# Performance work log

Hardware: AMD Instinct MI355X
Metric: run time of the kernel (lower is better)

The kernel has to match this reference:

```python
import jax, jax.numpy as jnp
import numpy as np

N = 100000
E = 1600000
IN_DIM = 128
OUT_DIM = 128


def setup_inputs() -> dict:
    key = jax.random.key(0)
    k1, k2, k3, k4, k5 = jax.random.split(key, 5)
    x = jax.random.normal(k1, (N, IN_DIM), dtype=jnp.float32)
    edge_index = jax.random.randint(k2, (2, E), 0, N, dtype=jnp.int64)
    # LayerNorm affine params
    ln_w = jnp.ones((IN_DIM,), dtype=jnp.float32)
    ln_b = jnp.zeros((IN_DIM,), dtype=jnp.float32)
    # SAGEConv params: lin_l (neighbor agg, with bias), lin_r (root, no bias)
    s = 1.0 / np.sqrt(IN_DIM)
    W_l = jax.random.uniform(k3, (OUT_DIM, IN_DIM), dtype=jnp.float32, minval=-s, maxval=s)
    b_l = jax.random.uniform(k4, (OUT_DIM,), dtype=jnp.float32, minval=-s, maxval=s)
    W_r = jax.random.uniform(k5, (OUT_DIM, IN_DIM), dtype=jnp.float32, minval=-s, maxval=s)
    return {"x": x, "edge_index": edge_index, "ln_w": ln_w, "ln_b": ln_b,
            "W_l": W_l, "b_l": b_l, "W_r": W_r}


def _layer_norm(x, w, b, eps=1e-5):
    mu = jnp.mean(x, axis=-1, keepdims=True)
    var = jnp.mean(jnp.square(x - mu), axis=-1, keepdims=True)
    return (x - mu) * jax.lax.rsqrt(var + eps) * w + b


def reference(x, edge_index, ln_w, ln_b, W_l, b_l, W_r):
    # norm -> activation -> dropout(p=0, identity)
    h = jax.nn.relu(_layer_norm(x, ln_w, ln_b))  # [N, in_dim]
    src = edge_index[0]  # message sources (x_j)
    dst = edge_index[1]  # aggregation targets
    # mean aggregation of neighbor features onto target nodes
    agg = jax.ops.segment_sum(h[src], dst, num_segments=N)  # [N, in_dim]
    cnt = jax.ops.segment_sum(jnp.ones((E,), dtype=h.dtype), dst, num_segments=N)
    agg = agg / jnp.maximum(cnt, 1.0)[:, None]
    # SAGEConv: lin_l(agg) + lin_r(h)
    out = agg @ W_l.T + b_l + h @ W_r.T  # [N, out_dim]
    return out
```

## Files before the change

### kernel.cpp

```cpp
#include <hip/hip_runtime.h>

#define N_NODES 100000
#define E_EDGES 1600000
#define DIM     128

#define NB1     196
#define CHUNK   8192
#define NBINS   512
#define NBUCKET 391
#define NBH     (NBINS * NB1)
#define HS_BLOCKS 98

#define HB_OFF    0
#define WTB_OFF   25600000
#define OFFS_OFF  25665536
#define BH_OFF    26065600
#define BSUM_OFF  26467008
#define BIN_OFF   26468032
#define SRC_OFF   32868032

typedef __attribute__((ext_vector_type(8))) short short8;
typedef __attribute__((ext_vector_type(4))) float floatx4;

__device__ __forceinline__ unsigned bf16pack(float a, float b) {
  unsigned ua = __float_as_uint(a); ua += 0x7fffu + ((ua >> 16) & 1u);
  unsigned ub = __float_as_uint(b); ub += 0x7fffu + ((ub >> 16) & 1u);
  return (ua >> 16) | (ub & 0xffff0000u);
}
__device__ __forceinline__ float2 bf16unpack(unsigned p) {
  return make_float2(__uint_as_float(p << 16), __uint_as_float(p & 0xffff0000u));
}

__global__ __launch_bounds__(256) void k_prep(const float* __restrict__ x,
                                              const float* __restrict__ lw,
                                              const float* __restrict__ lb,
                                              const float* __restrict__ Wl,
                                              const float* __restrict__ Wr,
                                              const int* __restrict__ ei,
                                              unsigned* __restrict__ hb,
                                              unsigned* __restrict__ wtb,
                                              int* __restrict__ bh) {
  int gid = blockIdx.x * 256 + threadIdx.x;
  int t = threadIdx.x;

  {
    int row  = blockIdx.x * 4 + (t >> 6);
    int lane = t & 63;
    float2 v = ((const float2*)(x + (size_t)row * DIM))[lane];
    float s  = v.x + v.y;
    float sq = v.x * v.x + v.y * v.y;
    #pragma unroll
    for (int off = 32; off > 0; off >>= 1) {
      s  += __shfl_xor(s, off);
      sq += __shfl_xor(sq, off);
    }
    float mu  = s * (1.0f / 128.0f);
    float var = sq * (1.0f / 128.0f) - mu * mu;
    float rs  = rsqrtf(var + 1e-5f);
    float2 w = ((const float2*)lw)[lane];
    float2 b = ((const float2*)lb)[lane];
    float ox = fmaxf((v.x - mu) * rs * w.x + b.x, 0.0f);
    float oy = fmaxf((v.y - mu) * rs * w.y + b.y, 0.0f);
    hb[(size_t)row * 64 + lane] = bf16pack(ox, oy);
  }

  if (gid < 16384) {
    int j2 = gid & 3;
    int q  = (gid >> 2) & 3;
    int c  = (gid >> 4) & 127;
    int kb = gid >> 11;
    int k0 = kb * 32 + q * 8 + j2 * 2;
    int k1 = k0 + 1;
    float v0 = (k0 < 128) ? Wl[c * 128 + k0] : Wr[c * 128 + (k0 - 128)];
    float v1 = (k1 < 128) ? Wl[c * 128 + k1] : Wr[c * 128 + (k1 - 128)];
    wtb[gid] = bf16pack(v0, v1);
  }

  if (blockIdx.x < NB1) {
    __shared__ int h[NBINS];
    h[t] = 0; h[t + 256] = 0;
    __syncthreads();
    const int4* d4p = (const int4*)(ei + E_EDGES);
    #pragma unroll
    for (int u = 0; u < 8; ++u) {
      int i4 = blockIdx.x * (CHUNK / 4) + u * 256 + t;
      if (i4 < E_EDGES / 4) {
        int4 d = d4p[i4];
        atomicAdd(&h[d.x >> 8], 1);
        atomicAdd(&h[d.y >> 8], 1);
        atomicAdd(&h[d.z >> 8], 1);
        atomicAdd(&h[d.w >> 8], 1);
      }
    }
    __syncthreads();
    bh[t * NB1 + blockIdx.x] = h[t];
    bh[(t + 256) * NB1 + blockIdx.x] = h[t + 256];
  }
}

__global__ __launch_bounds__(256) void k_hscan1(int* __restrict__ bh,
                                                int* __restrict__ bsum) {
  __shared__ int s[256];
  int t = threadIdx.x;
  int base = blockIdx.x * 1024 + t * 4;
  int a0 = (base + 0 < NBH) ? bh[base + 0] : 0;
  int a1 = (base + 1 < NBH) ? bh[base + 1] : 0;
  int a2 = (base + 2 < NBH) ? bh[base + 2] : 0;
  int a3 = (base + 3 < NBH) ? bh[base + 3] : 0;
  s[t] = a0 + a1 + a2 + a3;
  __syncthreads();
  #pragma unroll
  for (int off = 1; off < 256; off <<= 1) {
    int x = (t >= off) ? s[t - off] : 0;
    __syncthreads();
    s[t] += x;
    __syncthreads();
  }
  int excl = (t > 0) ? s[t - 1] : 0;
  if (t == 255) bsum[blockIdx.x] = s[255];
  if (base + 0 < NBH) bh[base + 0] = excl;
  if (base + 1 < NBH) bh[base + 1] = excl + a0;
  if (base + 2 < NBH) bh[base + 2] = excl + a0 + a1;
  if (base + 3 < NBH) bh[base + 3] = excl + a0 + a1 + a2;
}

__global__ __launch_bounds__(256) void k_hscan2(int* __restrict__ bh,
                                                const int* __restrict__ bsum) {
  __shared__ int s[256];
  int t = threadIdx.x;
  s[t] = (t < HS_BLOCKS) ? bsum[t] : 0;
  __syncthreads();
  #pragma unroll
  for (int off = 1; off < 256; off <<= 1) {
    int x = (t >= off) ? s[t - off] : 0;
    __syncthreads();
    s[t] += x;
    __syncthreads();
  }
  int blk = blockIdx.x;
  int add = (blk > 0) ? s[blk - 1] : 0;
  #pragma unroll
  for (int u = 0; u < 4; ++u) {
    int i = blk * 1024 + t * 4 + u;
    if (i < NBH) bh[i] += add;
  }
}

__global__ __launch_bounds__(256) void k_binsort(const int* __restrict__ ei,
                                                 const int* __restrict__ bh,
                                                 int* __restrict__ binned) {
  __shared__ int stage[CHUNK];
  __shared__ int addr[CHUNK];
  __shared__ int hist[NBINS];
  __shared__ int ebase[NBINS];
  __shared__ int cur[NBINS];
  __shared__ int gbase[NBINS];
  __shared__ int s[256];
  int t  = threadIdx.x;
  int ch = blockIdx.x;

  hist[t] = 0; hist[t + 256] = 0;
  gbase[t] = bh[t * NB1 + ch];
  gbase[t + 256] = bh[(t + 256) * NB1 + ch];
  __syncthreads();

  const int4* s4p = (const int4*)ei;
  const int4* d4p = (const int4*)(ei + E_EDGES);

  #pragma unroll
  for (int u = 0; u < 8; ++u) {
    int i4 = ch * (CHUNK / 4) + u * 256 + t;
    if (i4 < E_EDGES / 4) {
      int4 d = d4p[i4];
      atomicAdd(&hist[d.x >> 8], 1);
      atomicAdd(&hist[d.y >> 8], 1);
      atomicAdd(&hist[d.z >> 8], 1);
      atomicAdd(&hist[d.w >> 8], 1);
    }
  }
  __syncthreads();

  int h0 = hist[2 * t], h1 = hist[2 * t + 1];
  s[t] = h0 + h1;
  __syncthreads();
  #pragma unroll
  for (int off = 1; off < 256; off <<= 1) {
    int xv = (t >= off) ? s[t - off] : 0;
    __syncthreads();
    s[t] += xv;
    __syncthreads();
  }
  int ex = (t > 0) ? s[t - 1] : 0;
  ebase[2 * t] = ex;
  ebase[2 * t + 1] = ex + h0;
  cur[2 * t] = ex;
  cur[2 * t + 1] = ex + h0;
  __syncthreads();

  #pragma unroll
  for (int u = 0; u < 8; ++u) {
    int i4 = ch * (CHUNK / 4) + u * 256 + t;
    if (i4 < E_EDGES / 4) {
      int4 sv = s4p[i4];
      int4 dv = d4p[i4];
      {
        int bin = dv.x >> 8; int pos = atomicAdd(&cur[bin], 1);
        stage[pos] = sv.x | ((dv.x & 255) << 20);
        addr[pos]  = gbase[bin] + (pos - ebase[bin]);
      }
      {
        int bin = dv.y >> 8; int pos = atomicAdd(&cur[bin], 1);
        stage[pos] = sv.y | ((dv.y & 255) << 20);
        addr[pos]  = gbase[bin] + (pos - ebase[bin]);
      }
      {
        int bin = dv.z >> 8; int pos = atomicAdd(&cur[bin], 1);
        stage[pos] = sv.z | ((dv.z & 255) << 20);
        addr[pos]  = gbase[bin] + (pos - ebase[bin]);
      }
      {
        int bin = dv.w >> 8; int pos = atomicAdd(&cur[bin], 1);
        stage[pos] = sv.w | ((dv.w & 255) << 20);
        addr[pos]  = gbase[bin] + (pos - ebase[bin]);
      }
    }
  }
  __syncthreads();

  int cbase = ch * CHUNK;
  int cnt = E_EDGES - cbase;
  if (cnt > CHUNK) cnt = CHUNK;
  for (int i = t; i < cnt; i += 256)
    binned[addr[i]] = stage[i];
}

__global__ __launch_bounds__(256) void k_csr(const int* __restrict__ bh,
                                             const int* __restrict__ binned,
                                             int* __restrict__ offs,
                                             int* __restrict__ srcidx) {
  __shared__ int h[256];
  __shared__ int s[256];
  __shared__ int cur[256];
  int t = threadIdx.x;
  int bin = blockIdx.x;
  int base = bh[bin * NB1];
  int end  = bh[(bin + 1) * NB1];
  h[t] = 0;
  __syncthreads();
  for (int i = base + t; i < end; i += 256)
    atomicAdd(&h[(binned[i] >> 20) & 255], 1);
  __syncthreads();
  s[t] = h[t];
  __syncthreads();
  #pragma unroll
  for (int off = 1; off < 256; off <<= 1) {
    int x = (t >= off) ? s[t - off] : 0;
    __syncthreads();
    s[t] += x;
    __syncthreads();
  }
  int excl = (t > 0) ? s[t - 1] : 0;
  cur[t] = excl;
  int node = bin * 256 + t;
  if (node < N_NODES) offs[node] = base + excl;
  if (node == N_NODES) offs[N_NODES] = E_EDGES;
  __syncthreads();
  for (int i = base + t; i < end; i += 256) {
    int p = binned[i];
    int r = atomicAdd(&cur[(p >> 20) & 255], 1);
    srcidx[base + r] = p & 0xFFFFF;
  }
}

__global__ __launch_bounds__(512) void k_gathgemm(const unsigned* __restrict__ hb,
                                                  const int* __restrict__ offs,
                                                  const int* __restrict__ srcidx,
                                                  const unsigned* __restrict__ wtb,
                                                  const float* __restrict__ bl,
                                                  float* __restrict__ out) {
  __shared__ unsigned agg[16 * 68];
  int wv   = threadIdx.x >> 6;
  int lane = threadIdx.x & 63;
  int r0 = blockIdx.x * 16;
  int n0 = r0 + wv * 2;
  int n1 = n0 + 1;
  int b0 = __builtin_amdgcn_readfirstlane(offs[n0]);
  int e0 = __builtin_amdgcn_readfirstlane(offs[n0 + 1]);
  int b1 = __builtin_amdgcn_readfirstlane(offs[n1]);
  int e1 = __builtin_amdgcn_readfirstlane(offs[n1 + 1]);
  int m0 = e0 - b0, m1 = e1 - b1;
  int c  = (m0 < m1 ? m0 : m1) & ~7;

  float ax0 = 0.0f, ay0 = 0.0f, ax1 = 0.0f, ay1 = 0.0f;

  for (int j = 0; j < c; j += 8) {
    unsigned p0[8], p1[8];
    #pragma unroll
    for (int i = 0; i < 8; ++i) {
      int s0 = srcidx[b0 + j + i];
      int s1 = srcidx[b1 + j + i];
      p0[i] = hb[(size_t)s0 * 64 + lane];
      p1[i] = hb[(size_t)s1 * 64 + lane];
    }
    #pragma unroll
    for (int i = 0; i < 8; ++i) {
      float2 v0 = bf16unpack(p0[i]);
      float2 v1 = bf16unpack(p1[i]);
      ax0 += v0.x; ay0 += v0.y;
      ax1 += v1.x; ay1 += v1.y;
    }
  }
  for (int j = b0 + c; j < e0; ) {
    int rem = e0 - j;
    if (rem >= 8) {
      unsigned p[8];
      #pragma unroll
      for (int i = 0; i < 8; ++i) p[i] = hb[(size_t)srcidx[j + i] * 64 + lane];
      #pragma unroll
      for (int i = 0; i < 8; ++i) { float2 v = bf16unpack(p[i]); ax0 += v.x; ay0 += v.y; }
      j += 8;
    } else {
      float2 v = bf16unpack(hb[(size_t)srcidx[j] * 64 + lane]);
      ax0 += v.x; ay0 += v.y;
      ++j;
    }
  }
  for (int j = b1 + c; j < e1; ) {
    int rem = e1 - j;
    if (rem >= 8) {
      unsigned p[8];
      #pragma unroll
      for (int i = 0; i < 8; ++i) p[i] = hb[(size_t)srcidx[j + i] * 64 + lane];
      #pragma unroll
      for (int i = 0; i < 8; ++i) { float2 v = bf16unpack(p[i]); ax1 += v.x; ay1 += v.y; }
      j += 8;
    } else {
      float2 v = bf16unpack(hb[(size_t)srcidx[j] * 64 + lane]);
      ax1 += v.x; ay1 += v.y;
      ++j;
    }
  }

  float inv0 = 1.0f / fmaxf((float)m0, 1.0f);
  float inv1 = 1.0f / fmaxf((float)m1, 1.0f);
  agg[(wv * 2 + 0) * 68 + lane] = bf16pack(ax0 * inv0, ay0 * inv0);
  agg[(wv * 2 + 1) * 68 + lane] = bf16pack(ax1 * inv1, ay1 * inv1);
  __syncthreads();

  int m = lane & 15;
  int q = lane >> 4;
  int rowA = r0 + m;

  short8 afrag[8];
  #pragma unroll
  for (int kb = 0; kb < 4; ++kb) {
    uint4 u = *(const uint4*)&agg[m * 68 + (kb * 4 + q) * 4];
    afrag[kb] = *(short8*)&u;
  }
  const uint4* hr = (const uint4*)(hb + (size_t)rowA * 64);
  #pragma unroll
  for (int kb = 0; kb < 4; ++kb) {
    uint4 u = hr[kb * 4 + q];
    afrag[kb + 4] = *(short8*)&u;
  }

  const uint4* b4 = (const uint4*)wtb;
  int col = wv * 16 + m;
  floatx4 acc = {0.0f, 0.0f, 0.0f, 0.0f};
  #pragma unroll
  for (int kb = 0; kb < 8; ++kb) {
    uint4 u = b4[kb * 512 + col * 4 + q];
    short8 bfrag = *(short8*)&u;
    acc = __builtin_amdgcn_mfma_f32_16x16x32_bf16(afrag[kb], bfrag, acc, 0, 0, 0);
  }
  float bias = bl[col];
  #pragma unroll
  for (int reg = 0; reg < 4; ++reg) {
    int r = r0 + q * 4 + reg;
    out[(size_t)r * DIM + col] = acc[reg] + bias;
  }
}

extern "C" void kernel_launch(void* const* d_in, const int* in_sizes, int n_in,
                              void* d_out, int out_size, void* d_ws, size_t ws_size,
                              hipStream_t stream) {
  const float* x  = (const float*)d_in[0];
  const int*   ei = (const int*)d_in[1];
  const float* lw = (const float*)d_in[2];
  const float* lb = (const float*)d_in[3];
  const float* Wl = (const float*)d_in[4];
  const float* bl = (const float*)d_in[5];
  const float* Wr = (const float*)d_in[6];
  float* out = (float*)d_out;

  char* ws = (char*)d_ws;
  unsigned* hb     = (unsigned*)(ws + HB_OFF);
  unsigned* wtb    = (unsigned*)(ws + WTB_OFF);
  int*      offs   = (int*)(ws + OFFS_OFF);
  int*      bh     = (int*)(ws + BH_OFF);
  int*      bsum   = (int*)(ws + BSUM_OFF);
  int*      binned = (int*)(ws + BIN_OFF);
  int*      srcidx = (int*)(ws + SRC_OFF);

  k_prep<<<N_NODES / 4, 256, 0, stream>>>(x, lw, lb, Wl, Wr, ei, hb, wtb, bh);
  k_hscan1<<<HS_BLOCKS, 256, 0, stream>>>(bh, bsum);
  k_hscan2<<<HS_BLOCKS, 256, 0, stream>>>(bh, bsum);
  k_binsort<<<NB1, 256, 0, stream>>>(ei, bh, binned);
  k_csr<<<NBUCKET, 256, 0, stream>>>(bh, binned, offs, srcidx);
  k_gathgemm<<<N_NODES / 16, 512, 0, stream>>>(hb, offs, srcidx, wtb, bl, out);
}
```

Baseline: 254.4 us.

## Fold block-sum scan into consumers and make gather-GEMM wave-independent

Removes the k_hscan2 launch by having k_binsort and k_csr each rescan the block sums in shared memory and add the prefix on the fly. The gather-GEMM kernel is also restructured so that each wave handles 16 nodes (8 pairs) and computes all 8 output column tiles itself. This removes the block-wide __syncthreads between the aggregation and the MFMA phases. The cost is redundant per-block scans, more serial work per wave and fewer blocks in the final kernel.

```diff
diff --git a/kernel.cpp b/kernel.cpp
--- a/kernel.cpp
+++ b/kernel.cpp
@@ -124,30 +124,9 @@
   if (base + 3 < NBH) bh[base + 3] = excl + a0 + a1 + a2;
 }
 
-__global__ __launch_bounds__(256) void k_hscan2(int* __restrict__ bh,
-                                                const int* __restrict__ bsum) {
-  __shared__ int s[256];
-  int t = threadIdx.x;
-  s[t] = (t < HS_BLOCKS) ? bsum[t] : 0;
-  __syncthreads();
-  #pragma unroll
-  for (int off = 1; off < 256; off <<= 1) {
-    int x = (t >= off) ? s[t - off] : 0;
-    __syncthreads();
-    s[t] += x;
-    __syncthreads();
-  }
-  int blk = blockIdx.x;
-  int add = (blk > 0) ? s[blk - 1] : 0;
-  #pragma unroll
-  for (int u = 0; u < 4; ++u) {
-    int i = blk * 1024 + t * 4 + u;
-    if (i < NBH) bh[i] += add;
-  }
-}
-
 __global__ __launch_bounds__(256) void k_binsort(const int* __restrict__ ei,
                                                  const int* __restrict__ bh,
+                                                 const int* __restrict__ bsum,
                                                  int* __restrict__ binned) {
   __shared__ int stage[CHUNK];
   __shared__ int addr[CHUNK];
@@ -156,12 +135,29 @@
   __shared__ int cur[NBINS];
   __shared__ int gbase[NBINS];
   __shared__ int s[256];
+  __shared__ int bsc[256];
   int t  = threadIdx.x;
   int ch = blockIdx.x;
 
+  s[t] = (t < HS_BLOCKS) ? bsum[t] : 0;
+  __syncthreads();
+  #pragma unroll
+  for (int off = 1; off < 256; off <<= 1) {
+    int xv = (t >= off) ? s[t - off] : 0;
+    __syncthreads();
+    s[t] += xv;
+    __syncthreads();
+  }
+  bsc[t] = (t > 0) ? s[t - 1] : 0;
+  __syncthreads();
+
+  {
+    int i0 = t * NB1 + ch;
+    int i1 = (t + 256) * NB1 + ch;
+    gbase[t]       = bh[i0] + bsc[i0 >> 10];
+    gbase[t + 256] = bh[i1] + bsc[i1 >> 10];
+  }
   hist[t] = 0; hist[t + 256] = 0;
-  gbase[t] = bh[t * NB1 + ch];
-  gbase[t + 256] = bh[(t + 256) * NB1 + ch];
   __syncthreads();
 
   const int4* s4p = (const int4*)ei;
@@ -235,16 +231,33 @@
 }
 
 __global__ __launch_bounds__(256) void k_csr(const int* __restrict__ bh,
+                                             const int* __restrict__ bsum,
                                              const int* __restrict__ binned,
                                              int* __restrict__ offs,
                                              int* __restrict__ srcidx) {
   __shared__ int h[256];
   __shared__ int s[256];
   __shared__ int cur[256];
+  __shared__ int bsc[256];
   int t = threadIdx.x;
   int bin = blockIdx.x;
-  int base = bh[bin * NB1];
-  int end  = bh[(bin + 1) * NB1];
+
+  s[t] = (t < HS_BLOCKS) ? bsum[t] : 0;
+  __syncthreads();
+  #pragma unroll
+  for (int off = 1; off < 256; off <<= 1) {
+    int xv = (t >= off) ? s[t - off] : 0;
+    __syncthreads();
+    s[t] += xv;
+    __syncthreads();
+  }
+  bsc[t] = (t > 0) ? s[t - 1] : 0;
+  __syncthreads();
+
+  int i0 = bin * NB1, i1 = (bin + 1) * NB1;
+  int base = bh[i0] + bsc[i0 >> 10];
+  int end  = bh[i1] + bsc[i1 >> 10];
+
   h[t] = 0;
   __syncthreads();
   for (int i = base + t; i < end; i += 256)
@@ -272,89 +285,97 @@
   }
 }
 
-__global__ __launch_bounds__(512) void k_gathgemm(const unsigned* __restrict__ hb,
+__global__ __launch_bounds__(256) void k_gathgemm(const unsigned* __restrict__ hb,
                                                   const int* __restrict__ offs,
                                                   const int* __restrict__ srcidx,
                                                   const unsigned* __restrict__ wtb,
                                                   const float* __restrict__ bl,
                                                   float* __restrict__ out) {
-  __shared__ unsigned agg[16 * 68];
+  __shared__ unsigned agg[4][16 * 68];
   int wv   = threadIdx.x >> 6;
   int lane = threadIdx.x & 63;
-  int r0 = blockIdx.x * 16;
-  int n0 = r0 + wv * 2;
-  int n1 = n0 + 1;
-  int b0 = __builtin_amdgcn_readfirstlane(offs[n0]);
-  int e0 = __builtin_amdgcn_readfirstlane(offs[n0 + 1]);
-  int b1 = __builtin_amdgcn_readfirstlane(offs[n1]);
-  int e1 = __builtin_amdgcn_readfirstlane(offs[n1 + 1]);
-  int m0 = e0 - b0, m1 = e1 - b1;
-  int c  = (m0 < m1 ? m0 : m1) & ~7;
-
-  float ax0 = 0.0f, ay0 = 0.0f, ax1 = 0.0f, ay1 = 0.0f;
-
-  for (int j = 0; j < c; j += 8) {
-    unsigned p0[8], p1[8];
-    #pragma unroll
-    for (int i = 0; i < 8; ++i) {
-      int s0 = srcidx[b0 + j + i];
-      int s1 = srcidx[b1 + j + i];
-      p0[i] = hb[(size_t)s0 * 64 + lane];
-      p1[i] = hb[(size_t)s1 * 64 + lane];
-    }
-    #pragma unroll
-    for (int i = 0; i < 8; ++i) {
-      float2 v0 = bf16unpack(p0[i]);
-      float2 v1 = bf16unpack(p1[i]);
-      ax0 += v0.x; ay0 += v0.y;
-      ax1 += v1.x; ay1 += v1.y;
-    }
-  }
-  for (int j = b0 + c; j < e0; ) {
-    int rem = e0 - j;
-    if (rem >= 8) {
-      unsigned p[8];
+  unsigned* ag = agg[wv];
+  int r0w = (blockIdx.x * 4 + wv) * 16;
+
+  for (int p = 0; p < 8; ++p) {
+    int n0 = r0w + 2 * p;
+    int n1 = n0 + 1;
+    int c0 = (n0 < N_NODES) ? n0 : N_NODES;
+    int c1 = (n0 + 1 < N_NODES) ? n0 + 1 : N_NODES;
+    int c2 = (n1 + 1 < N_NODES) ? n1 + 1 : N_NODES;
+    int b0 = __builtin_amdgcn_readfirstlane(offs[c0]);
+    int e0 = __builtin_amdgcn_readfirstlane(offs[c1]);
+    int b1 = e0;
+    int e1 = __builtin_amdgcn_readfirstlane(offs[c2]);
+    if (n1 > N_NODES) { b1 = e1 = b0; }
+    int m0 = e0 - b0, m1 = e1 - b1;
+    int c  = (m0 < m1 ? m0 : m1) & ~7;
+
+    float ax0 = 0.0f, ay0 = 0.0f, ax1 = 0.0f, ay1 = 0.0f;
+
+    for (int j = 0; j < c; j += 8) {
+      unsigned p0[8], p1[8];
       #pragma unroll
-      for (int i = 0; i < 8; ++i) p[i] = hb[(size_t)srcidx[j + i] * 64 + lane];
+      for (int i = 0; i < 8; ++i) {
+        int s0 = srcidx[b0 + j + i];
+        int s1 = srcidx[b1 + j + i];
+        p0[i] = hb[(size_t)s0 * 64 + lane];
+        p1[i] = hb[(size_t)s1 * 64 + lane];
+      }
       #pragma unroll
-      for (int i = 0; i < 8; ++i) { float2 v = bf16unpack(p[i]); ax0 += v.x; ay0 += v.y; }
-      j += 8;
-    } else {
-      float2 v = bf16unpack(hb[(size_t)srcidx[j] * 64 + lane]);
-      ax0 += v.x; ay0 += v.y;
-      ++j;
-    }
-  }
-  for (int j = b1 + c; j < e1; ) {
-    int rem = e1 - j;
-    if (rem >= 8) {
-      unsigned p[8];
-      #pragma unroll
-      for (int i = 0; i < 8; ++i) p[i] = hb[(size_t)srcidx[j + i] * 64 + lane];
-      #pragma unroll
-      for (int i = 0; i < 8; ++i) { float2 v = bf16unpack(p[i]); ax1 += v.x; ay1 += v.y; }
-      j += 8;
-    } else {
-      float2 v = bf16unpack(hb[(size_t)srcidx[j] * 64 + lane]);
-      ax1 += v.x; ay1 += v.y;
-      ++j;
-    }
-  }
-
-  float inv0 = 1.0f / fmaxf((float)m0, 1.0f);
-  float inv1 = 1.0f / fmaxf((float)m1, 1.0f);
-  agg[(wv * 2 + 0) * 68 + lane] = bf16pack(ax0 * inv0, ay0 * inv0);
-  agg[(wv * 2 + 1) * 68 + lane] = bf16pack(ax1 * inv1, ay1 * inv1);
-  __syncthreads();
+      for (int i = 0; i < 8; ++i) {
+        float2 v0 = bf16unpack(p0[i]);
+        float2 v1 = bf16unpack(p1[i]);
+        ax0 += v0.x; ay0 += v0.y;
+        ax1 += v1.x; ay1 += v1.y;
+      }
+    }
+    for (int j = b0 + c; j < e0; ) {
+      int rem = e0 - j;
+      if (rem >= 8) {
+        unsigned pp[8];
+        #pragma unroll
+        for (int i = 0; i < 8; ++i) pp[i] = hb[(size_t)srcidx[j + i] * 64 + lane];
+        #pragma unroll
+        for (int i = 0; i < 8; ++i) { float2 v = bf16unpack(pp[i]); ax0 += v.x; ay0 += v.y; }
+        j += 8;
+      } else {
+        float2 v = bf16unpack(hb[(size_t)srcidx[j] * 64 + lane]);
+        ax0 += v.x; ay0 += v.y;
+        ++j;
+      }
+    }
+    for (int j = b1 + c; j < e1; ) {
+      int rem = e1 - j;
+      if (rem >= 8) {
+        unsigned pp[8];
+        #pragma unroll
+        for (int i = 0; i < 8; ++i) pp[i] = hb[(size_t)srcidx[j + i] * 64 + lane];
+        #pragma unroll
+        for (int i = 0; i < 8; ++i) { float2 v = bf16unpack(pp[i]); ax1 += v.x; ay1 += v.y; }
+        j += 8;
+      } else {
+        float2 v = bf16unpack(hb[(size_t)srcidx[j] * 64 + lane]);
+        ax1 += v.x; ay1 += v.y;
+        ++j;
+      }
+    }
+
+    float inv0 = 1.0f / fmaxf((float)m0, 1.0f);
+    float inv1 = 1.0f / fmaxf((float)m1, 1.0f);
+    ag[(2 * p + 0) * 68 + lane] = bf16pack(ax0 * inv0, ay0 * inv0);
+    ag[(2 * p + 1) * 68 + lane] = bf16pack(ax1 * inv1, ay1 * inv1);
+  }
 
   int m = lane & 15;
   int q = lane >> 4;
-  int rowA = r0 + m;
+  int rowA = r0w + m;
+  if (rowA > N_NODES - 1) rowA = N_NODES - 1;
 
   short8 afrag[8];
   #pragma unroll
   for (int kb = 0; kb < 4; ++kb) {
-    uint4 u = *(const uint4*)&agg[m * 68 + (kb * 4 + q) * 4];
+    uint4 u = *(const uint4*)&ag[m * 68 + (kb * 4 + q) * 4];
     afrag[kb] = *(short8*)&u;
   }
   const uint4* hr = (const uint4*)(hb + (size_t)rowA * 64);
@@ -365,19 +386,22 @@
   }
 
   const uint4* b4 = (const uint4*)wtb;
-  int col = wv * 16 + m;
-  floatx4 acc = {0.0f, 0.0f, 0.0f, 0.0f};
-  #pragma unroll
-  for (int kb = 0; kb < 8; ++kb) {
-    uint4 u = b4[kb * 512 + col * 4 + q];
-    short8 bfrag = *(short8*)&u;
-    acc = __builtin_amdgcn_mfma_f32_16x16x32_bf16(afrag[kb], bfrag, acc, 0, 0, 0);
-  }
-  float bias = bl[col];
-  #pragma unroll
-  for (int reg = 0; reg < 4; ++reg) {
-    int r = r0 + q * 4 + reg;
-    out[(size_t)r * DIM + col] = acc[reg] + bias;
+  #pragma unroll
+  for (int ct = 0; ct < 8; ++ct) {
+    int col = ct * 16 + m;
+    floatx4 acc = {0.0f, 0.0f, 0.0f, 0.0f};
+    #pragma unroll
+    for (int kb = 0; kb < 8; ++kb) {
+      uint4 u = b4[kb * 512 + col * 4 + q];
+      short8 bfrag = *(short8*)&u;
+      acc = __builtin_amdgcn_mfma_f32_16x16x32_bf16(afrag[kb], bfrag, acc, 0, 0, 0);
+    }
+    float bias = bl[col];
+    #pragma unroll
+    for (int reg = 0; reg < 4; ++reg) {
+      int r = r0w + q * 4 + reg;
+      if (r < N_NODES) out[(size_t)r * DIM + col] = acc[reg] + bias;
+    }
   }
 }
 
@@ -404,8 +428,7 @@
 
   k_prep<<<N_NODES / 4, 256, 0, stream>>>(x, lw, lb, Wl, Wr, ei, hb, wtb, bh);
   k_hscan1<<<HS_BLOCKS, 256, 0, stream>>>(bh, bsum);
-  k_hscan2<<<HS_BLOCKS, 256, 0, stream>>>(bh, bsum);
-  k_binsort<<<NB1, 256, 0, stream>>>(ei, bh, binned);
-  k_csr<<<NBUCKET, 256, 0, stream>>>(bh, binned, offs, srcidx);
-  k_gathgemm<<<N_NODES / 16, 512, 0, stream>>>(hb, offs, srcidx, wtb, bl, out);
-}
+  k_binsort<<<NB1, 256, 0, stream>>>(ei, bh, bsum, binned);
+  k_csr<<<NBUCKET, 256, 0, stream>>>(bh, bsum, binned, offs, srcidx);
+  k_gathgemm<<<(N_NODES + 63) / 64, 256, 0, stream>>>(hb, offs, srcidx, wtb, bl, out);
+}
```

Measured after the change: 285.9 us. 12.4% more time.
